# Kernel optimization log

Hardware: AMD Instinct MI355X
Metric: run time of the kernel (lower is better)

## Reference

```python
import jax, jax.numpy as jnp
import numpy as np

K = 6                 # color-coding parameter; K-1 message-passing steps
N = 50000             # num nodes
E = 1600000           # num edges (avg degree 32)
F = 384               # num_node_features = K * 2**K


def setup_inputs() -> dict:
    key = jax.random.key(0)
    k1, k2, k3, k4, k5 = jax.random.split(key, 5)
    s = 1.0 / np.sqrt(F)
    x = jax.random.normal(k1, (N, F), dtype=jnp.float32)
    edge_index = jax.random.randint(k2, (2, E), 0, N, dtype=jnp.int32)
    batch = jnp.zeros((N,), dtype=jnp.int32)  # unused by forward, kept for signature parity
    W_rel = jax.random.normal(k3, (F, F), dtype=jnp.float32) * s   # GraphConv lin_rel weight
    W_root = jax.random.normal(k4, (F, F), dtype=jnp.float32) * s  # GraphConv lin_root weight
    W_lin = jax.random.normal(k5, (1, F), dtype=jnp.float32) * s   # readout linear (no bias)
    return {"x": x, "edge_index": edge_index, "batch": batch,
            "W_rel": W_rel, "W_root": W_root, "W_lin": W_lin}


def reference(x, edge_index, batch, W_rel, W_root, W_lin):
    src = edge_index[0]
    dst = edge_index[1]
    # K-1 iterations of PyG GraphConv(aggr='add', bias=False) + relu:
    #   out = segment_sum(x[src] -> dst) @ W_rel^T + x @ W_root^T
    for _ in range(K - 1):
        agg = jax.ops.segment_sum(x[src], dst, num_segments=N)  # [N, F]
        x = jax.nn.relu(agg @ W_rel.T + x @ W_root.T)
    # readout: Linear(F, 1, bias=False)
    return x @ W_lin.T  # [N, 1]
```

## Files before the change

kernel.cpp:

```cpp
#include <hip/hip_runtime.h>
#include <hip/hip_bf16.h>

#define NN 50000
#define EE 1600000
#define FF 384
#define MPAD 50048
#define NITER 5
#define EPB 6250
#define BCAP 220000
#define GRP 6250

typedef unsigned int u32;
typedef unsigned short u16;
typedef __attribute__((ext_vector_type(8))) short short8;
typedef __attribute__((ext_vector_type(4))) float f32x4;

typedef const __attribute__((address_space(1))) void* gptr_t;
typedef __attribute__((address_space(3))) void* lptr_t;

__device__ __forceinline__ float bf_lo(u32 u) {
  u32 v = u << 16;
  return __builtin_bit_cast(float, v);
}
__device__ __forceinline__ float bf_hi(u32 u) {
  u32 v = u & 0xFFFF0000u;
  return __builtin_bit_cast(float, v);
}
__device__ __forceinline__ u32 f2bf(float f) {
  u32 u = __builtin_bit_cast(u32, f);
  return (u + 0x7FFFu + ((u >> 16) & 1u)) >> 16;
}
__device__ __forceinline__ u32 pack2(float lo, float hi) {
  return f2bf(lo) | (f2bf(hi) << 16);
}
__device__ __forceinline__ void load16_lds(const void* g, void* l) {
  __builtin_amdgcn_global_load_lds((gptr_t)g, (lptr_t)l, 16, 0, 0);
}

__global__ void init_bcur_kernel(int* __restrict__ bcur) {
  if (threadIdx.x < 8) bcur[threadIdx.x] = threadIdx.x * BCAP;
}

__global__ __launch_bounds__(256) void bucket_scatter_kernel(
    const int* __restrict__ src, const int* __restrict__ dst,
    int* __restrict__ bcur, int* __restrict__ es_src, int* __restrict__ es_dst) {
  __shared__ int osrc[EPB];
  __shared__ int odst[EPB];
  __shared__ int h[8], lo8[8], gbase[8], c2[8];
  const int t = threadIdx.x;
  if (t < 8) { h[t] = 0; c2[t] = 0; }
  __syncthreads();
  const int e0 = blockIdx.x * EPB;
  for (int i = t; i < EPB; i += 256) {
    int d = dst[e0 + i];
    atomicAdd(&h[d / GRP], 1);
  }
  __syncthreads();
  if (t == 0) { int r = 0; for (int b = 0; b < 8; ++b) { lo8[b] = r; r += h[b]; } }
  __syncthreads();
  if (t < 8) gbase[t] = atomicAdd(&bcur[t], h[t]);
  __syncthreads();
  for (int i = t; i < EPB; i += 256) {
    int s = src[e0 + i], d = dst[e0 + i];
    int b = d / GRP;
    int p = lo8[b] + atomicAdd(&c2[b], 1);
    osrc[p] = s; odst[p] = d;
  }
  __syncthreads();
  for (int i = t; i < EPB; i += 256) {
    int b = 0;
    while (b < 7 && i >= lo8[b + 1]) ++b;
    int g = gbase[b] + (i - lo8[b]);
    es_src[g] = osrc[i];
    es_dst[g] = odst[i];
  }
}

__global__ __launch_bounds__(256) void hist_part_kernel(
    const int* __restrict__ es_dst, const int* __restrict__ bcur,
    int* __restrict__ part) {
  __shared__ int h[GRP];
  const int g = blockIdx.x >> 5;
  const int s = blockIdx.x & 31;
  const int lo = g * GRP;
  const int base = g * BCAP;
  const int n = bcur[g] - base;
  const int chunk = (n + 31) >> 5;
  const int i0 = s * chunk;
  int i1 = i0 + chunk; if (i1 > n) i1 = n;
  for (int i = threadIdx.x; i < GRP; i += 256) h[i] = 0;
  __syncthreads();
  for (int i = i0 + threadIdx.x; i < i1; i += 256)
    atomicAdd(&h[es_dst[base + i] - lo], 1);
  __syncthreads();
  int* po = part + (size_t)blockIdx.x * GRP;
  for (int i = threadIdx.x; i < GRP; i += 256) po[i] = h[i];
}

__global__ void reduce_kernel(int* __restrict__ part, int* __restrict__ cnt) {
  int r = blockIdx.x * 256 + threadIdx.x;
  if (r >= NN) return;
  int g = r / GRP, o = r - g * GRP;
  int* p = part + (size_t)(g * 32) * GRP + o;
  int run = 0;
#pragma unroll
  for (int s = 0; s < 32; ++s) {
    int v = p[(size_t)s * GRP];
    p[(size_t)s * GRP] = run;
    run += v;
  }
  cnt[r] = run;
}

__global__ void scan_kernel(const int* __restrict__ cnt, int* __restrict__ row_start) {
  __shared__ int wsum[4];
  const int CH = 196;
  int t = threadIdx.x;
  int lo = t * CH;
  int hi = lo + CH; if (hi > NN) hi = NN;
  int s = 0;
  int n4 = (hi - lo) >> 2;
  const int4* p = (const int4*)(cnt + lo);
  for (int i = 0; i < n4; ++i) { int4 c = p[i]; s += c.x + c.y + c.z + c.w; }
  int lane = t & 63, w = t >> 6;
  int v = s;
  for (int d = 1; d < 64; d <<= 1) { int u = __shfl_up(v, d, 64); if (lane >= d) v += u; }
  if (lane == 63) wsum[w] = v;
  __syncthreads();
  int run = v - s;
  for (int i = 0; i < w; ++i) run += wsum[i];
  int4* q1 = (int4*)(row_start + lo);
  for (int k = 0; k < n4; ++k) {
    int4 c = p[k];
    int4 o; o.x = run; o.y = run + c.x; o.z = o.y + c.y; o.w = o.z + c.z;
    run = o.w + c.w;
    q1[k] = o;
  }
  if (hi == NN && lo < NN) row_start[NN] = run;
}

__global__ __launch_bounds__(256) void scatter4_kernel(
    const int* __restrict__ es_src, const int* __restrict__ es_dst,
    const int* __restrict__ bcur, const int* __restrict__ row_start,
    const int* __restrict__ part, int* __restrict__ col) {
  __shared__ int cur[GRP];
  const int g = blockIdx.x >> 5;
  const int s = blockIdx.x & 31;
  const int lo = g * GRP;
  const int base = g * BCAP;
  const int n = bcur[g] - base;
  const int chunk = (n + 31) >> 5;
  const int i0 = s * chunk;
  int i1 = i0 + chunk; if (i1 > n) i1 = n;
  const int* po = part + (size_t)blockIdx.x * GRP;
  for (int i = threadIdx.x; i < GRP; i += 256)
    cur[i] = row_start[lo + i] + po[i];
  __syncthreads();
  for (int i = i0 + threadIdx.x; i < i1; i += 256) {
    int d = es_dst[base + i];
    int p = atomicAdd(&cur[d - lo], 1);
    col[p] = es_src[base + i];
  }
}

__global__ void convert_x_kernel(const float* __restrict__ xin, u16* __restrict__ xout) {
  size_t i = ((size_t)blockIdx.x * 256 + threadIdx.x) * 4;
  if (i >= (size_t)NN * FF) return;
  float4 f = *(const float4*)(xin + i);
  u32 o0 = pack2(f.x, f.y);
  u32 o1 = pack2(f.z, f.w);
  u32* q = (u32*)(xout + i);
  q[0] = o0; q[1] = o1;
}

__global__ void build_bt_kernel(const float* __restrict__ Wr, const float* __restrict__ Wt,
                                u16* __restrict__ Bt) {
  int i = blockIdx.x * 256 + threadIdx.x;
  if (i >= FF * 2 * FF) return;
  int n = i / (2 * FF);
  int k = i - n * (2 * FF);
  float v = (k < FF) ? Wr[n * FF + k] : Wt[n * FF + (k - FF)];
  Bt[i] = (u16)f2bf(v);
}

__global__ void spmm_pass_kernel(const u16* __restrict__ x, const int* __restrict__ rs,
                                 const int* __restrict__ col, u16* __restrict__ agg,
                                 const int fo) {
  int row = blockIdx.x * 4 + (threadIdx.x >> 6);
  int lane = threadIdx.x & 63;
  if (row >= NN) return;
  int j0 = rs[row], j1 = rs[row + 1];
  float alo = 0.f, ahi = 0.f;
  const u32* xw = (const u32*)x + fo + lane;
  int j = j0;
  for (; j + 8 <= j1; j += 8) {
    int s0 = col[j + 0], s1 = col[j + 1], s2 = col[j + 2], s3 = col[j + 3];
    int s4 = col[j + 4], s5 = col[j + 5], s6 = col[j + 6], s7 = col[j + 7];
    u32 u0 = xw[(size_t)s0 * 192];
    u32 u1 = xw[(size_t)s1 * 192];
    u32 u2 = xw[(size_t)s2 * 192];
    u32 u3 = xw[(size_t)s3 * 192];
    u32 u4 = xw[(size_t)s4 * 192];
    u32 u5 = xw[(size_t)s5 * 192];
    u32 u6 = xw[(size_t)s6 * 192];
    u32 u7 = xw[(size_t)s7 * 192];
    alo += bf_lo(u0) + bf_lo(u1) + bf_lo(u2) + bf_lo(u3) +
           bf_lo(u4) + bf_lo(u5) + bf_lo(u6) + bf_lo(u7);
    ahi += bf_hi(u0) + bf_hi(u1) + bf_hi(u2) + bf_hi(u3) +
           bf_hi(u4) + bf_hi(u5) + bf_hi(u6) + bf_hi(u7);
  }
  for (; j < j1; ++j) {
    u32 u = xw[(size_t)col[j] * 192];
    alo += bf_lo(u); ahi += bf_hi(u);
  }
  ((u32*)agg)[(size_t)row * 192 + fo + lane] = pack2(alo, ahi);
}

__global__ __launch_bounds__(512, 4) void gemm_kernel(
    const u16* __restrict__ Aagg, const u16* __restrict__ Ax,
    const u16* __restrict__ Bt, u16* __restrict__ Xout) {
  __shared__ __align__(16) u16 As[2][64 * 64];
  __shared__ __align__(16) u16 Bs[384 * 64];

  const int orig = blockIdx.x;
  const int xcd = orig & 7, idx = orig >> 3;
  const int wg = ((xcd < 6) ? xcd * 98 : 6 * 98 + (xcd - 6) * 97) + idx;
  const int m0 = wg * 64;

  const int tid = threadIdx.x;
  const int lane = tid & 63;
  const int w = tid >> 6;
  const int wr = w >> 2;
  const int wc = w & 3;

  f32x4 acc[2][6] = {};

#define STAGE_A(KT, BUF)                                                        \
  {                                                                             \
    const u16* Asrc_ = ((KT) < 6) ? Aagg : Ax;                                  \
    const int kbA_ = (((KT) < 6) ? (KT) : (KT)-6) << 7;                         \
    const int rA_ = tid >> 3;                                                   \
    const int bcA_ = (tid & 7) << 4;                                            \
    load16_lds((const char*)Asrc_ + (size_t)(m0 + rA_) * 768 + kbA_ +           \
                   (bcA_ ^ ((rA_ & 7) << 4)),                                   \
               (char*)&As[BUF][0] + tid * 16);                                  \
  }

#define STAGE_B(KT)                                                             \
  {                                                                             \
    const int kbB_ = (KT) << 7;                                                 \
    _Pragma("unroll")                                                           \
    for (int i = 0; i < 6; ++i) {                                               \
      const int c = tid + i * 512;                                              \
      const int rB_ = c >> 3;                                                   \
      const int bcB_ = (c & 7) << 4;                                            \
      load16_lds((const char*)Bt + (size_t)rB_ * 1536 + kbB_ +                  \
                     (bcB_ ^ ((rB_ & 7) << 4)),                                 \
                 (char*)&Bs[0] + c * 16);                                       \
    }                                                                           \
  }

  STAGE_A(0, 0);
  STAGE_B(0);
  __syncthreads();

  int buf = 0;
  for (int kt = 0; kt < 12; ++kt) {
    if (kt < 11) STAGE_A(kt + 1, buf ^ 1);
#pragma unroll
    for (int ks = 0; ks < 2; ++ks) {
      short8 af[2], bfm[6];
#pragma unroll
      for (int ni = 0; ni < 6; ++ni) {
        const int r = wc * 96 + ni * 16 + (lane & 15);
        const int bc = (ks * 64 + ((lane >> 4) << 4)) ^ ((r & 7) << 4);
        bfm[ni] = *(const short8*)((const char*)&Bs[0] + r * 128 + bc);
      }
#pragma unroll
      for (int mi = 0; mi < 2; ++mi) {
        const int r = wr * 32 + mi * 16 + (lane & 15);
        const int bc = (ks * 64 + ((lane >> 4) << 4)) ^ ((r & 7) << 4);
        af[mi] = *(const short8*)((const char*)&As[buf][0] + r * 128 + bc);
      }
#pragma unroll
      for (int mi = 0; mi < 2; ++mi)
#pragma unroll
        for (int ni = 0; ni < 6; ++ni)
          acc[mi][ni] = __builtin_amdgcn_mfma_f32_16x16x32_bf16(af[mi], bfm[ni], acc[mi][ni], 0, 0, 0);
    }
    __syncthreads();
    if (kt < 11) {
      STAGE_B(kt + 1);
      __syncthreads();
    }
    buf ^= 1;
  }

#pragma unroll
  for (int mi = 0; mi < 2; ++mi) {
#pragma unroll
    for (int r = 0; r < 4; ++r) {
      const int row = m0 + wr * 32 + mi * 16 + ((lane >> 4) << 2) + r;
      u16* orow = Xout + (size_t)row * FF + wc * 96 + (lane & 15);
#pragma unroll
      for (int ni = 0; ni < 6; ++ni) {
        float v = fmaxf(acc[mi][ni][r], 0.0f);
        orow[ni * 16] = (u16)f2bf(v);
      }
    }
  }
#undef STAGE_A
#undef STAGE_B
}

__global__ void readout_kernel(const u16* __restrict__ x, const float* __restrict__ wl,
                               float* __restrict__ out) {
  int row = blockIdx.x * 4 + (threadIdx.x >> 6);
  int lane = threadIdx.x & 63;
  if (row >= NN) return;
  const u32* p = (const u32*)(x + (size_t)row * FF) + lane * 3;
  u32 u0 = p[0], u1 = p[1], u2 = p[2];
  const float* w = wl + lane * 6;
  float s = bf_lo(u0) * w[0] + bf_hi(u0) * w[1] +
            bf_lo(u1) * w[2] + bf_hi(u1) * w[3] +
            bf_lo(u2) * w[4] + bf_hi(u2) * w[5];
#pragma unroll
  for (int off = 32; off > 0; off >>= 1) s += __shfl_down(s, off, 64);
  if (lane == 0) out[row] = s;
}

extern "C" void kernel_launch(void* const* d_in, const int* in_sizes, int n_in,
                              void* d_out, int out_size, void* d_ws, size_t ws_size,
                              hipStream_t stream) {
  const float* x_in = (const float*)d_in[0];
  const int* ei = (const int*)d_in[1];
  const float* W_rel = (const float*)d_in[3];
  const float* W_root = (const float*)d_in[4];
  const float* W_lin = (const float*)d_in[5];
  float* out = (float*)d_out;

  char* ws = (char*)d_ws;
  int* cnt = (int*)(ws);
  int* bcur = cnt + NN;
  int* row_start = (int*)(ws + 200064);
  int* col = (int*)(ws + 600192);
  u16* Bt = (u16*)(ws + 7000192);
  u16* agg = (u16*)(ws + 7590016);
  u16* x0 = (u16*)(ws + 46026880);
  u16* x1 = (u16*)(ws + 84463744);
  if (ws_size < (size_t)122900608) return;
  int* es_src = (int*)(ws + 7590016);
  int* es_dst = (int*)(ws + 7590016 + 7040000);
  int* part = (int*)(ws + 7590016 + 14080000);

  const int* esrc = ei;
  const int* edst = ei + EE;

  hipMemsetAsync(agg + (size_t)NN * FF, 0, (size_t)(MPAD - NN) * FF * sizeof(u16), stream);
  hipMemsetAsync(x0 + (size_t)NN * FF, 0, (size_t)(MPAD - NN) * FF * sizeof(u16), stream);
  hipMemsetAsync(x1 + (size_t)NN * FF, 0, (size_t)(MPAD - NN) * FF * sizeof(u16), stream);

  init_bcur_kernel<<<1, 64, 0, stream>>>(bcur);
  bucket_scatter_kernel<<<EE / EPB, 256, 0, stream>>>(esrc, edst, bcur, es_src, es_dst);
  hist_part_kernel<<<256, 256, 0, stream>>>(es_dst, bcur, part);
  reduce_kernel<<<(NN + 255) / 256, 256, 0, stream>>>(part, cnt);
  scan_kernel<<<1, 256, 0, stream>>>(cnt, row_start);
  scatter4_kernel<<<256, 256, 0, stream>>>(es_src, es_dst, bcur, row_start, part, col);
  convert_x_kernel<<<(NN * FF / 4 + 255) / 256, 256, 0, stream>>>(x_in, x0);
  build_bt_kernel<<<(FF * 2 * FF + 255) / 256, 256, 0, stream>>>(W_rel, W_root, Bt);

  u16* xs = x0;
  u16* xd = x1;
  for (int t = 0; t < NITER; ++t) {
    for (int p = 0; p < 3; ++p)
      spmm_pass_kernel<<<NN / 4, 256, 0, stream>>>(xs, row_start, col, agg, p * 64);
    gemm_kernel<<<MPAD / 64, 512, 0, stream>>>(agg, xs, Bt, xd);
    u16* tmp = xs; xs = xd; xd = tmp;
  }
  readout_kernel<<<NN / 4, 256, 0, stream>>>(xs, W_lin, out);
}
```

Measured before the change: 1.133 ms.

## Store features in 32-column slabs and gather SpMM in 12 slices per launch

Node features and aggregates move from row-major to a slab layout of 12 slices of 32 bf16 columns, each slab holding 64 bytes per row. The SpMM becomes one launch over 12 slices with 16 lanes per row, and neighbour indices are loaded cooperatively and broadcast with shuffles. The GEMM A-loads, output stores, conversion and readout are rewritten for the slab layout, and a small kernel zeroes the pad rows instead of memsets. The aim is a per-slice working set small enough to stay in cache during the random gathers, at the cost of 64-byte gather granularity and scattered 2-byte GEMM output stores.

```diff
diff --git a/kernel.cpp b/kernel.cpp
--- a/kernel.cpp
+++ b/kernel.cpp
@@ -9,6 +9,10 @@
 #define EPB 6250
 #define BCAP 220000
 #define GRP 6250
+#define RBLK 3125
+#define NSLICE 12
+#define SLABB 3203072
+#define SLABW 800768
 
 typedef unsigned int u32;
 typedef unsigned short u16;
@@ -163,14 +167,25 @@
   }
 }
 
-__global__ void convert_x_kernel(const float* __restrict__ xin, u16* __restrict__ xout) {
+__global__ void convert_x_kernel(const float* __restrict__ xin, u32* __restrict__ xp) {
   size_t i = ((size_t)blockIdx.x * 256 + threadIdx.x) * 4;
   if (i >= (size_t)NN * FF) return;
   float4 f = *(const float4*)(xin + i);
-  u32 o0 = pack2(f.x, f.y);
-  u32 o1 = pack2(f.z, f.w);
-  u32* q = (u32*)(xout + i);
-  q[0] = o0; q[1] = o1;
+  int row = (int)(i / FF);
+  int c = (int)(i - (size_t)row * FF);
+  int j = c >> 1;
+  u32* q = xp + (size_t)(j >> 4) * SLABW + (size_t)row * 16 + (j & 15);
+  q[0] = pack2(f.x, f.y);
+  q[1] = pack2(f.z, f.w);
+}
+
+__global__ void zero_pad_kernel(u32* __restrict__ a0, u32* __restrict__ a1,
+                                u32* __restrict__ a2) {
+  int i = blockIdx.x * 256 + threadIdx.x;
+  if (i >= 9216) return;
+  int s = i / 768, rem = i - s * 768;
+  size_t addr = (size_t)s * SLABW + (size_t)(NN + rem / 16) * 16 + (rem & 15);
+  a0[addr] = 0; a1[addr] = 0; a2[addr] = 0;
 }
 
 __global__ void build_bt_kernel(const float* __restrict__ Wr, const float* __restrict__ Wt,
@@ -183,37 +198,41 @@
   Bt[i] = (u16)f2bf(v);
 }
 
-__global__ void spmm_pass_kernel(const u16* __restrict__ x, const int* __restrict__ rs,
-                                 const int* __restrict__ col, u16* __restrict__ agg,
-                                 const int fo) {
-  int row = blockIdx.x * 4 + (threadIdx.x >> 6);
-  int lane = threadIdx.x & 63;
-  if (row >= NN) return;
-  int j0 = rs[row], j1 = rs[row + 1];
+__global__ __launch_bounds__(256) void spmm12_kernel(
+    const u32* __restrict__ xp, const int* __restrict__ rs,
+    const int* __restrict__ col, u32* __restrict__ agg) {
+  const int pass = blockIdx.x / RBLK;
+  const int rb = blockIdx.x - pass * RBLK;
+  const int lane = threadIdx.x & 63;
+  const int sl = lane & 15;
+  const int r = rb * 16 + (threadIdx.x >> 6) * 4 + (lane >> 4);
+
+  const int j0 = rs[r], j1 = rs[r + 1];
+  const u32* xw = xp + (size_t)pass * SLABW + sl;
   float alo = 0.f, ahi = 0.f;
-  const u32* xw = (const u32*)x + fo + lane;
+
   int j = j0;
-  for (; j + 8 <= j1; j += 8) {
-    int s0 = col[j + 0], s1 = col[j + 1], s2 = col[j + 2], s3 = col[j + 3];
-    int s4 = col[j + 4], s5 = col[j + 5], s6 = col[j + 6], s7 = col[j + 7];
-    u32 u0 = xw[(size_t)s0 * 192];
-    u32 u1 = xw[(size_t)s1 * 192];
-    u32 u2 = xw[(size_t)s2 * 192];
-    u32 u3 = xw[(size_t)s3 * 192];
-    u32 u4 = xw[(size_t)s4 * 192];
-    u32 u5 = xw[(size_t)s5 * 192];
-    u32 u6 = xw[(size_t)s6 * 192];
-    u32 u7 = xw[(size_t)s7 * 192];
-    alo += bf_lo(u0) + bf_lo(u1) + bf_lo(u2) + bf_lo(u3) +
-           bf_lo(u4) + bf_lo(u5) + bf_lo(u6) + bf_lo(u7);
-    ahi += bf_hi(u0) + bf_hi(u1) + bf_hi(u2) + bf_hi(u3) +
-           bf_hi(u4) + bf_hi(u5) + bf_hi(u6) + bf_hi(u7);
-  }
-  for (; j < j1; ++j) {
-    u32 u = xw[(size_t)col[j] * 192];
-    alo += bf_lo(u); ahi += bf_hi(u);
-  }
-  ((u32*)agg)[(size_t)row * 192 + fo + lane] = pack2(alo, ahi);
+  for (; j + 16 <= j1; j += 16) {
+    int colv = __builtin_nontemporal_load(col + j + sl);
+#pragma unroll
+    for (int k = 0; k < 16; ++k) {
+      int s = __shfl(colv, k, 16);
+      u32 u = xw[(size_t)s * 16];
+      alo += bf_lo(u); ahi += bf_hi(u);
+    }
+  }
+  if (j < j1) {
+    int idx = j + sl; if (idx >= j1) idx = j1 - 1;
+    int colv = __builtin_nontemporal_load(col + idx);
+    int n = j1 - j;
+    for (int k = 0; k < n; ++k) {
+      int s = __shfl(colv, k, 16);
+      u32 u = xw[(size_t)s * 16];
+      alo += bf_lo(u); ahi += bf_hi(u);
+    }
+  }
+  __builtin_nontemporal_store(pack2(alo, ahi),
+                              agg + (size_t)pass * SLABW + (size_t)r * 16 + sl);
 }
 
 __global__ __launch_bounds__(512, 4) void gemm_kernel(
@@ -237,12 +256,12 @@
 
 #define STAGE_A(KT, BUF)                                                        \
   {                                                                             \
-    const u16* Asrc_ = ((KT) < 6) ? Aagg : Ax;                                  \
-    const int kbA_ = (((KT) < 6) ? (KT) : (KT)-6) << 7;                         \
+    const u16* base_ = ((KT) < 6) ? Aagg : Ax;                                  \
+    const int sl2_ = (((KT) < 6) ? (KT) : (KT)-6) * 2;                          \
     const int rA_ = tid >> 3;                                                   \
-    const int bcA_ = (tid & 7) << 4;                                            \
-    load16_lds((const char*)Asrc_ + (size_t)(m0 + rA_) * 768 + kbA_ +           \
-                   (bcA_ ^ ((rA_ & 7) << 4)),                                   \
+    const int bp_ = ((tid & 7) << 4) ^ ((rA_ & 7) << 4);                        \
+    load16_lds((const char*)base_ + (size_t)(sl2_ + (bp_ >> 6)) * SLABB +       \
+                   (size_t)(m0 + rA_) * 64 + (bp_ & 63),                        \
                (char*)&As[BUF][0] + tid * 16);                                  \
   }
 
@@ -301,11 +320,12 @@
 #pragma unroll
     for (int r = 0; r < 4; ++r) {
       const int row = m0 + wr * 32 + mi * 16 + ((lane >> 4) << 2) + r;
-      u16* orow = Xout + (size_t)row * FF + wc * 96 + (lane & 15);
 #pragma unroll
       for (int ni = 0; ni < 6; ++ni) {
+        const int c = wc * 96 + ni * 16 + (lane & 15);
         float v = fmaxf(acc[mi][ni][r], 0.0f);
-        orow[ni * 16] = (u16)f2bf(v);
+        Xout[(size_t)(c >> 5) * (SLABB / 2) + (size_t)row * 32 + (c & 31)] =
+            (u16)f2bf(v);
       }
     }
   }
@@ -313,17 +333,19 @@
 #undef STAGE_B
 }
 
-__global__ void readout_kernel(const u16* __restrict__ x, const float* __restrict__ wl,
+__global__ void readout_kernel(const u32* __restrict__ xp, const float* __restrict__ wl,
                                float* __restrict__ out) {
   int row = blockIdx.x * 4 + (threadIdx.x >> 6);
   int lane = threadIdx.x & 63;
   if (row >= NN) return;
-  const u32* p = (const u32*)(x + (size_t)row * FF) + lane * 3;
-  u32 u0 = p[0], u1 = p[1], u2 = p[2];
-  const float* w = wl + lane * 6;
-  float s = bf_lo(u0) * w[0] + bf_hi(u0) * w[1] +
-            bf_lo(u1) * w[2] + bf_hi(u1) * w[3] +
-            bf_lo(u2) * w[4] + bf_hi(u2) * w[5];
+  float s = 0.f;
+#pragma unroll
+  for (int k = 0; k < 3; ++k) {
+    const int sb = k * 4 + (lane >> 4);
+    u32 u = xp[(size_t)sb * SLABW + (size_t)row * 16 + (lane & 15)];
+    const int f = 2 * (64 * k + lane);
+    s += bf_lo(u) * wl[f] + bf_hi(u) * wl[f + 1];
+  }
 #pragma unroll
   for (int off = 32; off > 0; off >>= 1) s += __shfl_down(s, off, 64);
   if (lane == 0) out[row] = s;
@@ -356,26 +378,22 @@
   const int* esrc = ei;
   const int* edst = ei + EE;
 
-  hipMemsetAsync(agg + (size_t)NN * FF, 0, (size_t)(MPAD - NN) * FF * sizeof(u16), stream);
-  hipMemsetAsync(x0 + (size_t)NN * FF, 0, (size_t)(MPAD - NN) * FF * sizeof(u16), stream);
-  hipMemsetAsync(x1 + (size_t)NN * FF, 0, (size_t)(MPAD - NN) * FF * sizeof(u16), stream);
-
   init_bcur_kernel<<<1, 64, 0, stream>>>(bcur);
   bucket_scatter_kernel<<<EE / EPB, 256, 0, stream>>>(esrc, edst, bcur, es_src, es_dst);
   hist_part_kernel<<<256, 256, 0, stream>>>(es_dst, bcur, part);
   reduce_kernel<<<(NN + 255) / 256, 256, 0, stream>>>(part, cnt);
   scan_kernel<<<1, 256, 0, stream>>>(cnt, row_start);
   scatter4_kernel<<<256, 256, 0, stream>>>(es_src, es_dst, bcur, row_start, part, col);
-  convert_x_kernel<<<(NN * FF / 4 + 255) / 256, 256, 0, stream>>>(x_in, x0);
+  convert_x_kernel<<<(NN * FF / 4 + 255) / 256, 256, 0, stream>>>(x_in, (u32*)x0);
   build_bt_kernel<<<(FF * 2 * FF + 255) / 256, 256, 0, stream>>>(W_rel, W_root, Bt);
+  zero_pad_kernel<<<36, 256, 0, stream>>>((u32*)agg, (u32*)x0, (u32*)x1);
 
   u16* xs = x0;
   u16* xd = x1;
   for (int t = 0; t < NITER; ++t) {
-    for (int p = 0; p < 3; ++p)
-      spmm_pass_kernel<<<NN / 4, 256, 0, stream>>>(xs, row_start, col, agg, p * 64);
-    gemm_kernel<<<MPAD / 64, 512, 0, stream>>>(agg, xs, Bt, xd);
+    spmm12_kernel<<<NSLICE * RBLK, 256, 0, stream>>>((const u32*)xs, row_start, col, (u32*)agg);
+    gemm_kernel<<<782, 512, 0, stream>>>(agg, xs, Bt, xd);
     u16* tmp = xs; xs = xd; xd = tmp;
   }
-  readout_kernel<<<NN / 4, 256, 0, stream>>>(xs, W_lin, out);
-}
+  readout_kernel<<<NN / 4, 256, 0, stream>>>((const u32*)xs, W_lin, out);
+}
```

Result: slower. 1.557 ms (+37.5%).
